# Performance work log

Measured on AMD Instinct MI355X. Metric: run time of the kernel, lower is better.

The kernel has to match this reference:

```python
import jax, jax.numpy as jnp
import numpy as np

N = 50000        # nodes per node type (user, item)
D_IN = 256       # node_in_dim
D_REL = 64       # rel_in_dim
K = 8            # num_heads
D_OUT = 32       # node_out_dim (per head); K*D_OUT = 256
D_RELOUT = 32    # rel_out_dim (per head)
E = 300000       # edges per relation direction
SLOPE = 0.2

# relations: 0 = user-rates->item, 1 = item-rated-by->user,
#            2 = user-clicks->item, 3 = item-clicked-by->user
STYPE = [0, 1, 0, 1]   # 0=user, 1=item
DTYPE = [1, 0, 1, 0]
REV   = [1, 0, 3, 2]
GROUP = [[0, 2], [1, 3], [0, 2], [1, 3]]  # relations sharing this relation's dtype


def setup_inputs() -> dict:
    key = jax.random.key(0)
    ks = jax.random.split(key, 16)
    feats = jax.random.normal(ks[0], (4, N, D_IN), jnp.float32)
    rel_feats = jax.random.normal(ks[1], (4, D_REL), jnp.float32)
    src_rates = jax.random.randint(ks[2], (E,), 0, N, jnp.int32)
    dst_rates = jax.random.randint(ks[3], (E,), 0, N, jnp.int32)
    src_clicks = jax.random.randint(ks[4], (E,), 0, N, jnp.int32)
    dst_clicks = jax.random.randint(ks[5], (E,), 0, N, jnp.int32)
    s = 0.05
    W_node = s * jax.random.normal(ks[6], (2, D_IN, K * D_OUT), jnp.float32)          # fc_node per ntype (no bias)
    Wr = s * jax.random.normal(ks[7], (4, D_REL, 2 * K * D_OUT), jnp.float32)         # fc_rel per etype (no bias)
    Wres = s * jax.random.normal(ks[8], (2, D_IN, K * D_OUT), jnp.float32)            # fc_res per ntype
    bres = s * jax.random.normal(ks[9], (2, K * D_OUT), jnp.float32)
    resw = jax.random.uniform(ks[10], (2,), jnp.float32)                              # res_weight per ntype
    rel_attn = s * jax.random.normal(ks[11], (4, K, D_OUT), jnp.float32)              # rel_attn per etype
    Wupd = s * jax.random.normal(ks[12], (4, D_REL, K * D_RELOUT), jnp.float32)       # fc_upd per etype
    bupd = s * jax.random.normal(ks[13], (4, K * D_RELOUT), jnp.float32)
    return dict(feats=feats, rel_feats=rel_feats, src_rates=src_rates, dst_rates=dst_rates,
                src_clicks=src_clicks, dst_clicks=dst_clicks, W_node=W_node, Wr=Wr,
                Wres=Wres, bres=bres, resw=resw, rel_attn=rel_attn, Wupd=Wupd, bupd=bupd)


def _leaky(x):
    return jnp.where(x >= 0, x, SLOPE * x)


def _rel_graph_conv(hs, hd, attn, src, dst):
    """GAT-style conv for one relation. hs,hd: (N,K,D_OUT); attn: (K,2*D_OUT)."""
    el = (hs * attn[:, :D_OUT]).sum(-1)                    # (N_src, K)
    er = (hd * attn[:, D_OUT:]).sum(-1)                    # (N_dst, K)
    e = _leaky(el[src] + er[dst])                          # (E, K)
    # edge softmax grouped by destination node
    m = jax.ops.segment_max(e, dst, num_segments=N)        # (N, K)
    m = jnp.where(jnp.isfinite(m), m, 0.0)                 # nodes with no incoming edges
    ex = jnp.exp(e - m[dst])
    z = jax.ops.segment_sum(ex, dst, num_segments=N)
    a = ex / z[dst]                                        # (E, K)
    msg = hs[src] * a[:, :, None]                          # (E, K, D_OUT)
    out = jax.ops.segment_sum(msg, dst, num_segments=N)    # (N, K, D_OUT)
    return jax.nn.relu(out.reshape(N, K * D_OUT))


def reference(feats, rel_feats, src_rates, dst_rates, src_clicks, dst_clicks,
              W_node, Wr, Wres, bres, resw, rel_attn, Wupd, bupd):
    srcs = [src_rates, dst_rates, src_clicks, dst_clicks]
    dsts = [dst_rates, src_rates, dst_clicks, src_clicks]

    node_rel = []
    for r in range(4):
        # feat_src = feats of stype nodes (stored under the reverse relation); feat_dst under r
        hs = (feats[REV[r]] @ W_node[STYPE[r]]).reshape(N, K, D_OUT)
        hd = (feats[r] @ W_node[DTYPE[r]]).reshape(N, K, D_OUT)
        attn = (rel_feats[r] @ Wr[r]).reshape(K, 2 * D_OUT)
        conv = _rel_graph_conv(hs, hd, attn, srcs[r], dsts[r])
        # residual per destination node type
        alpha = jax.nn.sigmoid(resw[DTYPE[r]])
        inherit = feats[r] @ Wres[DTYPE[r]] + bres[DTYPE[r]]
        node_rel.append(alpha * conv + (1.0 - alpha) * inherit)

    # cross-relation attention per relation (over relations sharing the same dtype)
    out_feats = []
    for r in range(4):
        h = jnp.stack([node_rel[i] for i in GROUP[r]], 0).reshape(len(GROUP[r]), N, K, D_OUT)
        scores = (rel_attn[r] * h).sum(-1, keepdims=True)           # (R, N, K, 1)
        w = jax.nn.softmax(_leaky(scores), axis=0)
        out_feats.append((w * h).sum(0).reshape(N, K * D_OUT))
    out_nodes = jnp.stack(out_feats, 0)                             # (4, N, K*D_OUT)

    rel_out = jnp.einsum('rd,rdo->ro', rel_feats, Wupd) + bupd      # (4, K*D_RELOUT)
    return out_nodes, rel_out
```

## Files before the change

kernel.cpp:

```cpp
#include <hip/hip_runtime.h>

typedef unsigned short u16;
typedef __bf16 bf16x8 __attribute__((ext_vector_type(8)));
typedef float f32x4 __attribute__((ext_vector_type(4)));

#define N_NODES 50000
#define N_EDGES 300000
#define NP      12800000
#define NE8     400000

#define WP_OFF    0L
#define ATTN_OFF  524288L
#define ALPHA_OFF 532480L
#define P_OFF     532544L
#define EL_OFF    102932544L
#define ER_OFF    109332544L
#define CNT_OFF   115732544L
#define CUR_OFF   116532544L
#define ROW_OFF   117332544L
#define BS_OFF    118132560L
#define COL_OFF   118135696L

__device__ __forceinline__ float bf2f(u16 u){
  union { unsigned int i; float f; } v; v.i = ((unsigned int)u) << 16; return v.f;
}
__device__ __forceinline__ u16 f2bf(float f){
  union { float f; unsigned int i; } v; v.f = f;
  unsigned int x = v.i;
  x += 0x7fffu + ((x >> 16) & 1u);
  return (u16)(x >> 16);
}
__device__ __forceinline__ float leaky(float x){ return x >= 0.f ? x : 0.2f * x; }

__global__ void small_k(const float* __restrict__ rel_feats, const float* __restrict__ Wr,
                        const float* __restrict__ Wupd, const float* __restrict__ bupd,
                        const float* __restrict__ resw,
                        float* __restrict__ attn, float* __restrict__ alpha,
                        float* __restrict__ out_tail){
  int r = blockIdx.x, t = threadIdx.x;
  for (int j = t; j < 512; j += 256){
    float s = 0.f;
    for (int d = 0; d < 64; ++d)
      s += rel_feats[r*64 + d] * Wr[(r*64 + d)*512 + j];
    attn[r*512 + j] = s;
  }
  {
    float s = 0.f;
    for (int d = 0; d < 64; ++d)
      s += rel_feats[r*64 + d] * Wupd[(r*64 + d)*256 + t];
    out_tail[r*256 + t] = s + bupd[r*256 + t];
  }
  if (r == 0 && t < 2) alpha[t] = 1.f / (1.f + __expf(-resw[t]));
}

__global__ void prepack_k(const float* __restrict__ Wn, const float* __restrict__ Wres,
                          u16* __restrict__ Wp){
  int tid = blockIdx.x*256 + threadIdx.x;
  int m = tid >> 16, rem = tid & 65535;
  int kt = rem >> 13, rem2 = rem & 8191;
  int n = rem2 >> 5, kk = rem2 & 31;
  const float* src = (m < 2) ? (Wn + m*65536) : (Wres + (m - 2)*65536);
  Wp[tid] = f2bf(src[(kt*32 + kk)*256 + n]);
}

__global__ __launch_bounds__(256, 4) void gemm_k(const float* __restrict__ feats,
                                              const u16* __restrict__ Wp,
                                              const float* __restrict__ bres,
                                              const float* __restrict__ alpha_ws,
                                              u16* __restrict__ Pbase, float* __restrict__ outbase,
                                              const float* __restrict__ attn,
                                              float* __restrict__ EL, float* __restrict__ ER){
  const int rel = blockIdx.y >> 1;
  const int mat = blockIdx.y & 1;
  const int dt = 1 - (rel & 1);
  const float* __restrict__ A = feats + (size_t)rel*NP;
  const u16*   __restrict__ W = Wp + (mat*2 + dt)*65536;

  const int tid = threadIdx.x;
  const int lane = tid & 63, wave = tid >> 6;
  const int quad = lane >> 4, n0 = lane & 15;
  const int wrow = blockIdx.x*64;
  const int cbase = wave*64;
  f32x4 acc[4][4];
#pragma unroll
  for (int f = 0; f < 4; ++f)
#pragma unroll
    for (int nt = 0; nt < 4; ++nt)
      acc[f][nt] = f32x4{0.f,0.f,0.f,0.f};

  for (int kt = 0; kt < 8; ++kt){
    const u16* bp = W + kt*8192 + (cbase + n0)*32 + quad*8;
    bf16x8 b[4];
#pragma unroll
    for (int nt = 0; nt < 4; ++nt)
      b[nt] = *(const bf16x8*)(bp + nt*512);
    bf16x8 af[4];
#pragma unroll
    for (int f = 0; f < 4; ++f){
      int row = wrow + f*16 + n0;
      if (row < N_NODES){
        const float* ap = A + (size_t)row*256 + kt*32 + quad*8;
        f32x4 a0 = *(const f32x4*)ap;
        f32x4 a1 = *(const f32x4*)(ap + 4);
#pragma unroll
        for (int j = 0; j < 4; ++j){ af[f][j] = (__bf16)a0[j]; af[f][4+j] = (__bf16)a1[j]; }
      } else {
#pragma unroll
        for (int j = 0; j < 8; ++j) af[f][j] = (__bf16)0.f;
      }
    }
#pragma unroll
    for (int f = 0; f < 4; ++f)
#pragma unroll
      for (int nt = 0; nt < 4; ++nt)
        acc[f][nt] = __builtin_amdgcn_mfma_f32_16x16x32_bf16(af[f], b[nt], acc[f][nt], 0, 0, 0);
  }

  if (mat == 1){
    float* __restrict__ out = outbase + (size_t)rel*NP;
    const float* __restrict__ bias = bres + dt*256;
    const float one_m_al = 1.f - alpha_ws[dt];
#pragma unroll
    for (int f = 0; f < 4; ++f)
#pragma unroll
      for (int nt = 0; nt < 4; ++nt){
        int col = cbase + nt*16 + n0;
        float bv = bias[col];
#pragma unroll
        for (int reg = 0; reg < 4; ++reg){
          int row = wrow + f*16 + quad*4 + reg;
          if (row < N_NODES)
            out[(size_t)row*256 + col] = one_m_al * (acc[f][nt][reg] + bv);
        }
      }
    return;
  }

  u16* __restrict__ Pout = Pbase + (size_t)rel*NP;
#pragma unroll
  for (int f = 0; f < 4; ++f)
#pragma unroll
    for (int nt = 0; nt < 4; ++nt){
      int col = cbase + nt*16 + n0;
#pragma unroll
      for (int reg = 0; reg < 4; ++reg){
        int row = wrow + f*16 + quad*4 + reg;
        if (row < N_NODES)
          Pout[(size_t)row*256 + col] = f2bf(acc[f][nt][reg]);
      }
    }

  const float* __restrict__ attnL = attn + (rel ^ 1)*512;
  const float* __restrict__ attnR = attn + rel*512 + 32;
  float* __restrict__ ELb = EL + (size_t)(rel ^ 1)*NE8;
  float* __restrict__ ERb = ER + (size_t)rel*NE8;
  const int h0 = 2*wave, h1 = 2*wave + 1;
  const float aL00 = attnL[h0*64 + n0], aL01 = attnL[h0*64 + 16 + n0];
  const float aL10 = attnL[h1*64 + n0], aL11 = attnL[h1*64 + 16 + n0];
  const float aR00 = attnR[h0*64 + n0], aR01 = attnR[h0*64 + 16 + n0];
  const float aR10 = attnR[h1*64 + n0], aR11 = attnR[h1*64 + 16 + n0];
#pragma unroll
  for (int f = 0; f < 4; ++f){
#pragma unroll
    for (int reg = 0; reg < 4; ++reg){
      float e0 = acc[f][0][reg]*aL00 + acc[f][1][reg]*aL01;
      float e1 = acc[f][2][reg]*aL10 + acc[f][3][reg]*aL11;
      float r0 = acc[f][0][reg]*aR00 + acc[f][1][reg]*aR01;
      float r1 = acc[f][2][reg]*aR10 + acc[f][3][reg]*aR11;
      e0 += __shfl_xor(e0, 1); e0 += __shfl_xor(e0, 2); e0 += __shfl_xor(e0, 4); e0 += __shfl_xor(e0, 8);
      e1 += __shfl_xor(e1, 1); e1 += __shfl_xor(e1, 2); e1 += __shfl_xor(e1, 4); e1 += __shfl_xor(e1, 8);
      r0 += __shfl_xor(r0, 1); r0 += __shfl_xor(r0, 2); r0 += __shfl_xor(r0, 4); r0 += __shfl_xor(r0, 8);
      r1 += __shfl_xor(r1, 1); r1 += __shfl_xor(r1, 2); r1 += __shfl_xor(r1, 4); r1 += __shfl_xor(r1, 8);
      int row = wrow + f*16 + quad*4 + reg;
      if (row < N_NODES){
        if (n0 == 0)      ELb[row*8 + h0] = e0;
        else if (n0 == 1) ELb[row*8 + h1] = e1;
        else if (n0 == 2) ERb[row*8 + h0] = r0;
        else if (n0 == 3) ERb[row*8 + h1] = r1;
      }
    }
  }
}

__global__ void zero_k(int* __restrict__ p, int n){
  int i = blockIdx.x*256 + threadIdx.x; if (i < n) p[i] = 0;
}
__global__ void hist_k(const int* __restrict__ sr, const int* __restrict__ dr,
                       const int* __restrict__ sc, const int* __restrict__ dc,
                       int* __restrict__ counts){
  int r = blockIdx.y; int e = blockIdx.x*256 + threadIdx.x;
  if (e >= N_EDGES) return;
  const int* dst = (r == 0) ? dr : (r == 1) ? sr : (r == 2) ? dc : sc;
  atomicAdd(&counts[r*N_NODES + dst[e]], 1);
}
__global__ void scan1_k(const int* __restrict__ counts, int* __restrict__ rowptr,
                        int* __restrict__ bsums){
  int r = blockIdx.y; int i = blockIdx.x*256 + threadIdx.x;
  int lane = threadIdx.x & 63, wave = threadIdx.x >> 6;
  int v = (i < N_NODES) ? counts[r*N_NODES + i] : 0;
  int orig = v;
  for (int off = 1; off < 64; off <<= 1){ int t = __shfl_up(v, off); if (lane >= off) v += t; }
  __shared__ int wsum[4];
  if (lane == 63) wsum[wave] = v;
  __syncthreads();
  int add = 0;
  for (int w = 0; w < wave; ++w) add += wsum[w];
  v += add;
  if (i < N_NODES) rowptr[r*(N_NODES+1) + i] = v - orig;
  if (threadIdx.x == 255) bsums[r*196 + blockIdx.x] = v;
}
__global__ void scan2_k(int* __restrict__ bsums){
  int lane = threadIdx.x & 63, r = threadIdx.x >> 6;
  int carry = 0;
  for (int c = 0; c < 4; ++c){
    int i = c*64 + lane;
    int v = (i < 196) ? bsums[r*196 + i] : 0;
    int orig = v;
    for (int off = 1; off < 64; off <<= 1){ int t = __shfl_up(v, off); if (lane >= off) v += t; }
    int excl = v - orig + carry;
    if (i < 196) bsums[r*196 + i] = excl;
    carry += __shfl(v, 63);
  }
}
__global__ void scan3_k(const int* __restrict__ bsums, int* __restrict__ rowptr){
  int r = blockIdx.y; int i = blockIdx.x*256 + threadIdx.x;
  if (i < N_NODES) rowptr[r*(N_NODES+1) + i] += bsums[r*196 + blockIdx.x];
  if (i == N_NODES) rowptr[r*(N_NODES+1) + N_NODES] = N_EDGES;
}
__global__ void scatter_k(const int* __restrict__ sr, const int* __restrict__ dr,
                          const int* __restrict__ sc, const int* __restrict__ dc,
                          const int* __restrict__ rowptr, int* __restrict__ cur,
                          int* __restrict__ colsrc){
  int r = blockIdx.y; int e = blockIdx.x*256 + threadIdx.x;
  if (e >= N_EDGES) return;
  const int* dst = (r == 0) ? dr : (r == 1) ? sr : (r == 2) ? dc : sc;
  const int* src = (r == 0) ? sr : (r == 1) ? dr : (r == 2) ? sc : dc;
  int d = dst[e];
  int pos = rowptr[r*(N_NODES+1) + d] + atomicAdd(&cur[r*N_NODES + d], 1);
  colsrc[r*N_EDGES + pos] = src[e];
}

__global__ __launch_bounds__(256) void aggcross_k(
    const int* __restrict__ rowptr, const int* __restrict__ colsrc,
    const float* __restrict__ EL, const float* __restrict__ ER,
    const u16* __restrict__ P, const float* __restrict__ rel_attn,
    const float* __restrict__ alpha_ws, float* __restrict__ out){
  const int g = blockIdx.y;
  const int wave = threadIdx.x >> 6, lane = threadIdx.x & 63;
  const int n = blockIdx.x*4 + wave;
  if (n >= N_NODES) return;
  const int k0 = lane >> 3, j = lane & 7;
  const float al = alpha_ws[g ^ 1];
  f32x4 h[2];
#pragma unroll
  for (int which = 0; which < 2; ++which){
    const int r = g + which*2;
    const int rp0 = rowptr[r*(N_NODES+1) + n], rp1 = rowptr[r*(N_NODES+1) + n + 1];
    const float er = ER[(size_t)r*NE8 + n*8 + k0];
    const float* el = EL + (size_t)r*NE8;
    const int* cs = colsrc + r*N_EDGES;
    const u16* Ps = P + (size_t)(r ^ 1)*NP;

    float z = 0.f, a0 = 0.f, a1 = 0.f, a2 = 0.f, a3 = 0.f;
    for (int base = rp0; base < rp1; base += 8){
      const int cnt = rp1 - base;
      const int m = cnt < 8 ? cnt : 8;
      int sj = cs[base + (j < m ? j : 0)];
      float x = leaky(el[sj*8 + k0] + er);
      float p = (j < m) ? __expf(x - 10.f) : 0.f;
      ushort4 hv[8]; float pv[8];
#pragma unroll
      for (int t = 0; t < 8; ++t){
        if (t < m){
          int s = __shfl(sj, t);
          hv[t] = *(const ushort4*)(Ps + (size_t)s*256 + lane*4);
          pv[t] = __shfl(p, (lane & 56) | t);
        }
      }
#pragma unroll
      for (int t = 0; t < 8; ++t){
        if (t < m){
          float q = pv[t];
          z += q;
          a0 += q*bf2f(hv[t].x); a1 += q*bf2f(hv[t].y);
          a2 += q*bf2f(hv[t].z); a3 += q*bf2f(hv[t].w);
        }
      }
    }
    float inv = (rp1 > rp0) ? 1.f / z : 0.f;
    f32x4 inh = *(const f32x4*)(out + (size_t)r*NP + (size_t)n*256 + lane*4);
    h[which][0] = al * fmaxf(a0*inv, 0.f) + inh[0];
    h[which][1] = al * fmaxf(a1*inv, 0.f) + inh[1];
    h[which][2] = al * fmaxf(a2*inv, 0.f) + inh[2];
    h[which][3] = al * fmaxf(a3*inv, 0.f) + inh[3];
  }
#pragma unroll
  for (int which = 0; which < 2; ++which){
    int rr = g + which*2;
    const float* ra = rel_attn + rr*256 + k0*32 + j*4;
    float s0 = 0.f, s1 = 0.f;
#pragma unroll
    for (int jj = 0; jj < 4; ++jj){
      float a = ra[jj];
      s0 += a * h[0][jj]; s1 += a * h[1][jj];
    }
    s0 += __shfl_xor(s0, 1); s1 += __shfl_xor(s1, 1);
    s0 += __shfl_xor(s0, 2); s1 += __shfl_xor(s1, 2);
    s0 += __shfl_xor(s0, 4); s1 += __shfl_xor(s1, 4);
    float l0 = leaky(s0), l1 = leaky(s1);
    float mx = fmaxf(l0, l1);
    float e0 = __expf(l0 - mx), e1 = __expf(l1 - mx);
    float w0 = e0 / (e0 + e1), w1 = 1.f - w0;
    f32x4 o;
#pragma unroll
    for (int jj = 0; jj < 4; ++jj) o[jj] = w0*h[0][jj] + w1*h[1][jj];
    *(f32x4*)(out + ((size_t)rr*N_NODES + n)*256 + lane*4) = o;
  }
}

extern "C" void kernel_launch(void* const* d_in, const int* in_sizes, int n_in,
                              void* d_out, int out_size, void* d_ws, size_t ws_size,
                              hipStream_t stream) {
  (void)in_sizes; (void)n_in; (void)out_size; (void)ws_size;
  const float* feats      = (const float*)d_in[0];
  const float* rel_feats  = (const float*)d_in[1];
  const int*   src_rates  = (const int*)d_in[2];
  const int*   dst_rates  = (const int*)d_in[3];
  const int*   src_clicks = (const int*)d_in[4];
  const int*   dst_clicks = (const int*)d_in[5];
  const float* W_node     = (const float*)d_in[6];
  const float* Wr         = (const float*)d_in[7];
  const float* Wres       = (const float*)d_in[8];
  const float* bres       = (const float*)d_in[9];
  const float* resw       = (const float*)d_in[10];
  const float* rel_attn   = (const float*)d_in[11];
  const float* Wupd       = (const float*)d_in[12];
  const float* bupd       = (const float*)d_in[13];

  char* w = (char*)d_ws;
  u16*   Wp     = (u16*)(w + WP_OFF);
  float* attn   = (float*)(w + ATTN_OFF);
  float* alpha  = (float*)(w + ALPHA_OFF);
  u16*   P      = (u16*)(w + P_OFF);
  float* EL     = (float*)(w + EL_OFF);
  float* ER     = (float*)(w + ER_OFF);
  int*   counts = (int*)(w + CNT_OFF);
  int*   cur    = (int*)(w + CUR_OFF);
  int*   rowptr = (int*)(w + ROW_OFF);
  int*   bsums  = (int*)(w + BS_OFF);
  int*   colsrc = (int*)(w + COL_OFF);
  float* out    = (float*)d_out;

  zero_k<<<1563, 256, 0, stream>>>(counts, 400000);
  small_k<<<4, 256, 0, stream>>>(rel_feats, Wr, Wupd, bupd, resw, attn, alpha,
                                 out + (size_t)4*NP);
  prepack_k<<<1024, 256, 0, stream>>>(W_node, Wres, Wp);

  hist_k<<<dim3(1172, 4), 256, 0, stream>>>(src_rates, dst_rates, src_clicks, dst_clicks, counts);
  scan1_k<<<dim3(196, 4), 256, 0, stream>>>(counts, rowptr, bsums);
  scan2_k<<<1, 256, 0, stream>>>(bsums);
  scan3_k<<<dim3(196, 4), 256, 0, stream>>>(bsums, rowptr);
  scatter_k<<<dim3(1172, 4), 256, 0, stream>>>(src_rates, dst_rates, src_clicks, dst_clicks,
                                               rowptr, cur, colsrc);

  gemm_k<<<dim3(782, 8), 256, 0, stream>>>(feats, Wp, bres, alpha, P, out, attn, EL, ER);

  aggcross_k<<<dim3(12500, 2), 256, 0, stream>>>(rowptr, colsrc, EL, ER, P,
                                                 rel_attn, alpha, out);
}
```

Measured before the change: 928.3 us.

## Fuse both weight GEMMs per block and merge setup kernels

```diff
diff --git a/kernel.cpp b/kernel.cpp
--- a/kernel.cpp
+++ b/kernel.cpp
@@ -32,159 +32,165 @@
 }
 __device__ __forceinline__ float leaky(float x){ return x >= 0.f ? x : 0.2f * x; }
 
-__global__ void small_k(const float* __restrict__ rel_feats, const float* __restrict__ Wr,
+__global__ void setup_k(const float* __restrict__ rel_feats, const float* __restrict__ Wr,
                         const float* __restrict__ Wupd, const float* __restrict__ bupd,
                         const float* __restrict__ resw,
+                        const float* __restrict__ Wn, const float* __restrict__ Wres,
+                        int* __restrict__ zp, u16* __restrict__ Wp,
                         float* __restrict__ attn, float* __restrict__ alpha,
                         float* __restrict__ out_tail){
-  int r = blockIdx.x, t = threadIdx.x;
-  for (int j = t; j < 512; j += 256){
-    float s = 0.f;
-    for (int d = 0; d < 64; ++d)
-      s += rel_feats[r*64 + d] * Wr[(r*64 + d)*512 + j];
-    attn[r*512 + j] = s;
+  const int bx = blockIdx.x, t = threadIdx.x;
+  if (bx < 1563){
+    int i = bx*256 + t; if (i < 400000) zp[i] = 0;
+    return;
+  }
+  if (bx < 2587){
+    int tid = (bx - 1563)*256 + t;
+    int m = tid >> 16, rem = tid & 65535;
+    int kt = rem >> 13, rem2 = rem & 8191;
+    int n = rem2 >> 5, kk = rem2 & 31;
+    const float* src = (m < 2) ? (Wn + m*65536) : (Wres + (m - 2)*65536);
+    Wp[tid] = f2bf(src[(kt*32 + kk)*256 + n]);
+    return;
   }
   {
-    float s = 0.f;
-    for (int d = 0; d < 64; ++d)
-      s += rel_feats[r*64 + d] * Wupd[(r*64 + d)*256 + t];
-    out_tail[r*256 + t] = s + bupd[r*256 + t];
-  }
-  if (r == 0 && t < 2) alpha[t] = 1.f / (1.f + __expf(-resw[t]));
-}
-
-__global__ void prepack_k(const float* __restrict__ Wn, const float* __restrict__ Wres,
-                          u16* __restrict__ Wp){
-  int tid = blockIdx.x*256 + threadIdx.x;
-  int m = tid >> 16, rem = tid & 65535;
-  int kt = rem >> 13, rem2 = rem & 8191;
-  int n = rem2 >> 5, kk = rem2 & 31;
-  const float* src = (m < 2) ? (Wn + m*65536) : (Wres + (m - 2)*65536);
-  Wp[tid] = f2bf(src[(kt*32 + kk)*256 + n]);
-}
-
-__global__ __launch_bounds__(256, 4) void gemm_k(const float* __restrict__ feats,
+    int r = bx - 2587;
+    for (int j = t; j < 512; j += 256){
+      float s = 0.f;
+      for (int d = 0; d < 64; ++d)
+        s += rel_feats[r*64 + d] * Wr[(r*64 + d)*512 + j];
+      attn[r*512 + j] = s;
+    }
+    {
+      float s = 0.f;
+      for (int d = 0; d < 64; ++d)
+        s += rel_feats[r*64 + d] * Wupd[(r*64 + d)*256 + t];
+      out_tail[r*256 + t] = s + bupd[r*256 + t];
+    }
+    if (r == 0 && t < 2) alpha[t] = 1.f / (1.f + __expf(-resw[t]));
+  }
+}
+
+__global__ __launch_bounds__(256, 6) void gemm_k(const float* __restrict__ feats,
                                               const u16* __restrict__ Wp,
                                               const float* __restrict__ bres,
                                               const float* __restrict__ alpha_ws,
                                               u16* __restrict__ Pbase, float* __restrict__ outbase,
                                               const float* __restrict__ attn,
                                               float* __restrict__ EL, float* __restrict__ ER){
-  const int rel = blockIdx.y >> 1;
-  const int mat = blockIdx.y & 1;
+  const int rel = blockIdx.y;
   const int dt = 1 - (rel & 1);
   const float* __restrict__ A = feats + (size_t)rel*NP;
-  const u16*   __restrict__ W = Wp + (mat*2 + dt)*65536;
 
   const int tid = threadIdx.x;
   const int lane = tid & 63, wave = tid >> 6;
   const int quad = lane >> 4, n0 = lane & 15;
-  const int wrow = blockIdx.x*64;
+  const int wrow = blockIdx.x*32;
   const int cbase = wave*64;
-  f32x4 acc[4][4];
-#pragma unroll
-  for (int f = 0; f < 4; ++f)
-#pragma unroll
-    for (int nt = 0; nt < 4; ++nt)
-      acc[f][nt] = f32x4{0.f,0.f,0.f,0.f};
-
-  for (int kt = 0; kt < 8; ++kt){
-    const u16* bp = W + kt*8192 + (cbase + n0)*32 + quad*8;
-    bf16x8 b[4];
-#pragma unroll
-    for (int nt = 0; nt < 4; ++nt)
-      b[nt] = *(const bf16x8*)(bp + nt*512);
-    bf16x8 af[4];
-#pragma unroll
-    for (int f = 0; f < 4; ++f){
-      int row = wrow + f*16 + n0;
-      if (row < N_NODES){
-        const float* ap = A + (size_t)row*256 + kt*32 + quad*8;
-        f32x4 a0 = *(const f32x4*)ap;
-        f32x4 a1 = *(const f32x4*)(ap + 4);
-#pragma unroll
-        for (int j = 0; j < 4; ++j){ af[f][j] = (__bf16)a0[j]; af[f][4+j] = (__bf16)a1[j]; }
-      } else {
-#pragma unroll
-        for (int j = 0; j < 8; ++j) af[f][j] = (__bf16)0.f;
+
+#pragma unroll
+  for (int mat = 0; mat < 2; ++mat){
+    const u16* __restrict__ W = Wp + (mat*2 + dt)*65536;
+    f32x4 acc[2][4];
+#pragma unroll
+    for (int f = 0; f < 2; ++f)
+#pragma unroll
+      for (int nt = 0; nt < 4; ++nt)
+        acc[f][nt] = f32x4{0.f,0.f,0.f,0.f};
+
+    for (int kt = 0; kt < 8; ++kt){
+      const u16* bp = W + kt*8192 + (cbase + n0)*32 + quad*8;
+      bf16x8 b[4];
+#pragma unroll
+      for (int nt = 0; nt < 4; ++nt)
+        b[nt] = *(const bf16x8*)(bp + nt*512);
+      bf16x8 af[2];
+#pragma unroll
+      for (int f = 0; f < 2; ++f){
+        int row = wrow + f*16 + n0;
+        if (row < N_NODES){
+          const float* ap = A + (size_t)row*256 + kt*32 + quad*8;
+          f32x4 a0 = *(const f32x4*)ap;
+          f32x4 a1 = *(const f32x4*)(ap + 4);
+#pragma unroll
+          for (int j = 0; j < 4; ++j){ af[f][j] = (__bf16)a0[j]; af[f][4+j] = (__bf16)a1[j]; }
+        } else {
+#pragma unroll
+          for (int j = 0; j < 8; ++j) af[f][j] = (__bf16)0.f;
+        }
       }
-    }
-#pragma unroll
-    for (int f = 0; f < 4; ++f)
-#pragma unroll
-      for (int nt = 0; nt < 4; ++nt)
-        acc[f][nt] = __builtin_amdgcn_mfma_f32_16x16x32_bf16(af[f], b[nt], acc[f][nt], 0, 0, 0);
-  }
-
-  if (mat == 1){
-    float* __restrict__ out = outbase + (size_t)rel*NP;
-    const float* __restrict__ bias = bres + dt*256;
-    const float one_m_al = 1.f - alpha_ws[dt];
-#pragma unroll
-    for (int f = 0; f < 4; ++f)
-#pragma unroll
-      for (int nt = 0; nt < 4; ++nt){
-        int col = cbase + nt*16 + n0;
-        float bv = bias[col];
+#pragma unroll
+      for (int f = 0; f < 2; ++f)
+#pragma unroll
+        for (int nt = 0; nt < 4; ++nt)
+          acc[f][nt] = __builtin_amdgcn_mfma_f32_16x16x32_bf16(af[f], b[nt], acc[f][nt], 0, 0, 0);
+    }
+
+    if (mat == 1){
+      float* __restrict__ out = outbase + (size_t)rel*NP;
+      const float* __restrict__ bias = bres + dt*256;
+      const float one_m_al = 1.f - alpha_ws[dt];
+#pragma unroll
+      for (int f = 0; f < 2; ++f)
+#pragma unroll
+        for (int nt = 0; nt < 4; ++nt){
+          int col = cbase + nt*16 + n0;
+          float bv = bias[col];
+#pragma unroll
+          for (int reg = 0; reg < 4; ++reg){
+            int row = wrow + f*16 + quad*4 + reg;
+            if (row < N_NODES)
+              out[(size_t)row*256 + col] = one_m_al * (acc[f][nt][reg] + bv);
+          }
+        }
+    } else {
+      u16* __restrict__ Pout = Pbase + (size_t)rel*NP;
+#pragma unroll
+      for (int f = 0; f < 2; ++f)
+#pragma unroll
+        for (int nt = 0; nt < 4; ++nt){
+          int col = cbase + nt*16 + n0;
+#pragma unroll
+          for (int reg = 0; reg < 4; ++reg){
+            int row = wrow + f*16 + quad*4 + reg;
+            if (row < N_NODES)
+              Pout[(size_t)row*256 + col] = f2bf(acc[f][nt][reg]);
+          }
+        }
+      const float* __restrict__ attnL = attn + (rel ^ 1)*512;
+      const float* __restrict__ attnR = attn + rel*512 + 32;
+      float* __restrict__ ELb = EL + (size_t)(rel ^ 1)*NE8;
+      float* __restrict__ ERb = ER + (size_t)rel*NE8;
+      const int h0 = 2*wave, h1 = 2*wave + 1;
+      const float aL00 = attnL[h0*64 + n0], aL01 = attnL[h0*64 + 16 + n0];
+      const float aL10 = attnL[h1*64 + n0], aL11 = attnL[h1*64 + 16 + n0];
+      const float aR00 = attnR[h0*64 + n0], aR01 = attnR[h0*64 + 16 + n0];
+      const float aR10 = attnR[h1*64 + n0], aR11 = attnR[h1*64 + 16 + n0];
+#pragma unroll
+      for (int f = 0; f < 2; ++f){
 #pragma unroll
         for (int reg = 0; reg < 4; ++reg){
+          float e0 = acc[f][0][reg]*aL00 + acc[f][1][reg]*aL01;
+          float e1 = acc[f][2][reg]*aL10 + acc[f][3][reg]*aL11;
+          float r0 = acc[f][0][reg]*aR00 + acc[f][1][reg]*aR01;
+          float r1 = acc[f][2][reg]*aR10 + acc[f][3][reg]*aR11;
+          e0 += __shfl_xor(e0, 1); e0 += __shfl_xor(e0, 2); e0 += __shfl_xor(e0, 4); e0 += __shfl_xor(e0, 8);
+          e1 += __shfl_xor(e1, 1); e1 += __shfl_xor(e1, 2); e1 += __shfl_xor(e1, 4); e1 += __shfl_xor(e1, 8);
+          r0 += __shfl_xor(r0, 1); r0 += __shfl_xor(r0, 2); r0 += __shfl_xor(r0, 4); r0 += __shfl_xor(r0, 8);
+          r1 += __shfl_xor(r1, 1); r1 += __shfl_xor(r1, 2); r1 += __shfl_xor(r1, 4); r1 += __shfl_xor(r1, 8);
           int row = wrow + f*16 + quad*4 + reg;
-          if (row < N_NODES)
-            out[(size_t)row*256 + col] = one_m_al * (acc[f][nt][reg] + bv);
+          if (row < N_NODES){
+            if (n0 == 0)      ELb[row*8 + h0] = e0;
+            else if (n0 == 1) ELb[row*8 + h1] = e1;
+            else if (n0 == 2) ERb[row*8 + h0] = r0;
+            else if (n0 == 3) ERb[row*8 + h1] = r1;
+          }
         }
       }
-    return;
-  }
-
-  u16* __restrict__ Pout = Pbase + (size_t)rel*NP;
-#pragma unroll
-  for (int f = 0; f < 4; ++f)
-#pragma unroll
-    for (int nt = 0; nt < 4; ++nt){
-      int col = cbase + nt*16 + n0;
-#pragma unroll
-      for (int reg = 0; reg < 4; ++reg){
-        int row = wrow + f*16 + quad*4 + reg;
-        if (row < N_NODES)
-          Pout[(size_t)row*256 + col] = f2bf(acc[f][nt][reg]);
-      }
-    }
-
-  const float* __restrict__ attnL = attn + (rel ^ 1)*512;
-  const float* __restrict__ attnR = attn + rel*512 + 32;
-  float* __restrict__ ELb = EL + (size_t)(rel ^ 1)*NE8;
-  float* __restrict__ ERb = ER + (size_t)rel*NE8;
-  const int h0 = 2*wave, h1 = 2*wave + 1;
-  const float aL00 = attnL[h0*64 + n0], aL01 = attnL[h0*64 + 16 + n0];
-  const float aL10 = attnL[h1*64 + n0], aL11 = attnL[h1*64 + 16 + n0];
-  const float aR00 = attnR[h0*64 + n0], aR01 = attnR[h0*64 + 16 + n0];
-  const float aR10 = attnR[h1*64 + n0], aR11 = attnR[h1*64 + 16 + n0];
-#pragma unroll
-  for (int f = 0; f < 4; ++f){
-#pragma unroll
-    for (int reg = 0; reg < 4; ++reg){
-      float e0 = acc[f][0][reg]*aL00 + acc[f][1][reg]*aL01;
-      float e1 = acc[f][2][reg]*aL10 + acc[f][3][reg]*aL11;
-      float r0 = acc[f][0][reg]*aR00 + acc[f][1][reg]*aR01;
-      float r1 = acc[f][2][reg]*aR10 + acc[f][3][reg]*aR11;
-      e0 += __shfl_xor(e0, 1); e0 += __shfl_xor(e0, 2); e0 += __shfl_xor(e0, 4); e0 += __shfl_xor(e0, 8);
-      e1 += __shfl_xor(e1, 1); e1 += __shfl_xor(e1, 2); e1 += __shfl_xor(e1, 4); e1 += __shfl_xor(e1, 8);
-      r0 += __shfl_xor(r0, 1); r0 += __shfl_xor(r0, 2); r0 += __shfl_xor(r0, 4); r0 += __shfl_xor(r0, 8);
-      r1 += __shfl_xor(r1, 1); r1 += __shfl_xor(r1, 2); r1 += __shfl_xor(r1, 4); r1 += __shfl_xor(r1, 8);
-      int row = wrow + f*16 + quad*4 + reg;
-      if (row < N_NODES){
-        if (n0 == 0)      ELb[row*8 + h0] = e0;
-        else if (n0 == 1) ELb[row*8 + h1] = e1;
-        else if (n0 == 2) ERb[row*8 + h0] = r0;
-        else if (n0 == 3) ERb[row*8 + h1] = r1;
-      }
-    }
-  }
-}
-
-__global__ void zero_k(int* __restrict__ p, int n){
-  int i = blockIdx.x*256 + threadIdx.x; if (i < n) p[i] = 0;
-}
+    }
+  }
+}
+
 __global__ void hist_k(const int* __restrict__ sr, const int* __restrict__ dr,
                        const int* __restrict__ sc, const int* __restrict__ dc,
                        int* __restrict__ counts){
@@ -351,10 +357,8 @@
   int*   colsrc = (int*)(w + COL_OFF);
   float* out    = (float*)d_out;
 
-  zero_k<<<1563, 256, 0, stream>>>(counts, 400000);
-  small_k<<<4, 256, 0, stream>>>(rel_feats, Wr, Wupd, bupd, resw, attn, alpha,
-                                 out + (size_t)4*NP);
-  prepack_k<<<1024, 256, 0, stream>>>(W_node, Wres, Wp);
+  setup_k<<<2591, 256, 0, stream>>>(rel_feats, Wr, Wupd, bupd, resw, W_node, Wres,
+                                    counts, Wp, attn, alpha, out + (size_t)4*NP);
 
   hist_k<<<dim3(1172, 4), 256, 0, stream>>>(src_rates, dst_rates, src_clicks, dst_clicks, counts);
   scan1_k<<<dim3(196, 4), 256, 0, stream>>>(counts, rowptr, bsums);
@@ -363,7 +367,7 @@
   scatter_k<<<dim3(1172, 4), 256, 0, stream>>>(src_rates, dst_rates, src_clicks, dst_clicks,
                                                rowptr, cur, colsrc);
 
-  gemm_k<<<dim3(782, 8), 256, 0, stream>>>(feats, Wp, bres, alpha, P, out, attn, EL, ER);
+  gemm_k<<<dim3(1563, 4), 256, 0, stream>>>(feats, Wp, bres, alpha, P, out, attn, EL, ER);
 
   aggcross_k<<<dim3(12500, 2), 256, 0, stream>>>(rowptr, colsrc, EL, ER, P,
                                                  rel_attn, alpha, out);
```

Result: slower. 1.066 ms (+14.8%).
